# Optimization experiments

Measured on AMD Instinct MI355X. Metric: run time of the kernel, lower is better.

Reference implementation:

```python
import math
import jax, jax.numpy as jnp
import numpy as np

N, C_S, C_Z, C, H, PQK, PV = 768, 384, 128, 16, 12, 4, 8
INF, EPS = 100000.0, 1e-8


def _quat_to_rot(q):
    # q: [N,4] normalized quaternions -> [N,3,3] rotation matrices
    w, x, y, z = q[:, 0], q[:, 1], q[:, 2], q[:, 3]
    return jnp.stack([
        jnp.stack([1 - 2 * (y * y + z * z), 2 * (x * y - w * z), 2 * (x * z + w * y)], -1),
        jnp.stack([2 * (x * y + w * z), 1 - 2 * (x * x + z * z), 2 * (y * z - w * x)], -1),
        jnp.stack([2 * (x * z - w * y), 2 * (y * z + w * x), 1 - 2 * (x * x + y * y)], -1),
    ], -2)


def setup_inputs() -> dict:
    key = jax.random.key(0)
    ks = jax.random.split(key, 16)
    quat = jax.random.normal(ks[2], (N, 4))
    quat = quat / jnp.linalg.norm(quat, axis=-1, keepdims=True)
    sc = 0.02
    return {
        "s": jax.random.normal(ks[0], (N, C_S), jnp.float32),
        "z": jax.random.normal(ks[1], (N, N, C_Z), jnp.float32),
        "rot": _quat_to_rot(quat).astype(jnp.float32),
        "trans": jax.random.normal(ks[3], (N, 3), jnp.float32),
        "mask": jnp.ones((N,), jnp.float32),
        "Wq": sc * jax.random.normal(ks[4], (C_S, H * C), jnp.float32),
        "bq": jnp.zeros((H * C,), jnp.float32),
        "Wqp": sc * jax.random.normal(ks[5], (C_S, H * 3 * PQK), jnp.float32),
        "bqp": jnp.zeros((H * 3 * PQK,), jnp.float32),
        "Wkv": sc * jax.random.normal(ks[6], (C_S, 2 * H * C), jnp.float32),
        "bkv": jnp.zeros((2 * H * C,), jnp.float32),
        "Wkvp": sc * jax.random.normal(ks[7], (C_S, H * 3 * (PQK + PV)), jnp.float32),
        "bkvp": jnp.zeros((H * 3 * (PQK + PV),), jnp.float32),
        "Wb": sc * jax.random.normal(ks[8], (C_Z, H), jnp.float32),
        "bb": jnp.zeros((H,), jnp.float32),
        "head_weights": 0.5413 * jnp.ones((H,), jnp.float32),  # softplus^{-1}(1)
        "Wout": sc * jax.random.normal(ks[9], (H * (C_Z + C + PV * 4), C_S), jnp.float32),
        "bout": jnp.zeros((C_S,), jnp.float32),
    }


def _proj_points(x, W, b, rot, trans, P):
    # PointProjection: split last dim into 3 coord chunks, stack as last axis
    pl = x @ W + b                                   # [N, H*3*P]
    pl = pl.reshape(-1, 3, H * P).transpose(0, 2, 1).reshape(-1, H, P, 3)
    return jnp.einsum('nij,nhpj->nhpi', rot, pl) + trans[:, None, None, :]


def reference(s, z, rot, trans, mask, Wq, bq, Wqp, bqp, Wkv, bkv, Wkvp, bkvp,
              Wb, bb, head_weights, Wout, bout):
    q = (s @ Wq + bq).reshape(N, H, C)
    kv = (s @ Wkv + bkv).reshape(N, H, 2 * C)
    k, v = kv[..., :C], kv[..., C:]
    q_pts = _proj_points(s, Wqp, bqp, rot, trans, PQK)          # [N,H,PQK,3]
    kv_pts = _proj_points(s, Wkvp, bkvp, rot, trans, PQK + PV)  # [N,H,PQK+PV,3]
    k_pts, v_pts = kv_pts[..., :PQK, :], kv_pts[..., PQK:, :]

    b_bias = z @ Wb + bb                                        # [N,N,H]
    a = jnp.einsum('qhc,khc->hqk', q, k) * math.sqrt(1.0 / (3 * C))
    a = a + math.sqrt(1.0 / 3) * jnp.transpose(b_bias, (2, 0, 1))

    # point-distance attention: [q,k,H,PQK]
    d2 = jnp.sum((q_pts[:, None] - k_pts[None]) ** 2, axis=-1)
    hw = jax.nn.softplus(head_weights) * math.sqrt(1.0 / (3 * (PQK * 9.0 / 2)))
    pt_att = -0.5 * jnp.sum(d2 * hw[:, None], axis=-1)          # [q,k,H]
    a = a + jnp.transpose(pt_att, (2, 0, 1))

    sq_mask = INF * (mask[:, None] * mask[None, :] - 1.0)       # [q,k]
    a = jax.nn.softmax(a + sq_mask[None], axis=-1)              # [H,q,k]

    o = jnp.einsum('hqk,khc->qhc', a, v).reshape(N, H * C)
    o_pt = jnp.einsum('hqk,khpd->qhpd', a, v_pts)               # [q,H,PV,3]
    o_pt = jnp.einsum('nji,nhpj->nhpi', rot, o_pt - trans[:, None, None, :])  # invert_apply
    o_pt_norm = jnp.sqrt(jnp.sum(o_pt ** 2, -1) + EPS).reshape(N, H * PV)
    o_pt_flat = o_pt.reshape(N, H * PV, 3)
    o_pair = jnp.einsum('hqk,qkc->qhc', a, z).reshape(N, H * C_Z)

    cat = jnp.concatenate(
        [o, o_pt_flat[..., 0], o_pt_flat[..., 1], o_pt_flat[..., 2], o_pt_norm, o_pair], -1)
    return cat @ Wout + bout
```

## Files before the change

kernel.cpp:

```cpp
#include <hip/hip_runtime.h>
#include <math.h>

#define NN    768
#define CS    384
#define INF_  100000.0f

typedef __attribute__((ext_vector_type(8))) short s16x8;
typedef __attribute__((ext_vector_type(4))) float f32x4;

#define OFF_Q       0
#define OFF_K       147456
#define OFF_V       294912
#define OFF_QPRAW   442368
#define OFF_KVPRAW  552960
#define OFF_QPTS    884736
#define OFF_KPTS    995328
#define OFF_VPTS    1105920
#define OFF_KT      1327104
#define OFF_KPT     1474560
#define OFF_S       1585152
#define OFF_CAT     8414208

__device__ __forceinline__ unsigned short f2bf(float x) {
  unsigned u = __float_as_uint(x) + 0x8000u;
  return (unsigned short)(u >> 16);
}
__device__ __forceinline__ unsigned pk2(float a, float b) {
  return (unsigned)f2bf(a) | ((unsigned)f2bf(b) << 16);
}
__device__ __forceinline__ float bf2f(unsigned short u) {
  return __uint_as_float(((unsigned)u) << 16);
}

__global__ void __launch_bounds__(256)
k1_proj(const float* __restrict__ s,
        const float* __restrict__ Wq,  const float* __restrict__ bq,
        const float* __restrict__ Wqp, const float* __restrict__ bqp,
        const float* __restrict__ Wkv, const float* __restrict__ bkv,
        const float* __restrict__ Wkvp,const float* __restrict__ bkvp,
        float* __restrict__ ws) {
  const int n0 = blockIdx.x * 16;
  const int m0 = blockIdx.y * 128;
  const int t  = threadIdx.x;

  const float* W; const float* bv; int base, ncols;
  if (n0 < 192)      { W = Wq;   bv = bq;   base = 0;   ncols = 192; }
  else if (n0 < 576) { W = Wkv;  bv = bkv;  base = 192; ncols = 384; }
  else if (n0 < 720) { W = Wqp;  bv = bqp;  base = 576; ncols = 144; }
  else               { W = Wkvp; bv = bkvp; base = 720; ncols = 432; }
  const int jj0 = n0 - base;

  __shared__ float As[32 * 130];
  __shared__ float Bs[32 * 20];
  const int tx = t & 3, ty = t >> 2;
  float acc[2][4] = {{0.f}};

  for (int kc = 0; kc < CS; kc += 32) {
    __syncthreads();
    #pragma unroll
    for (int jj = 0; jj < 4; ++jj) {
      const int idx = t + 256 * jj;
      const int row = idx >> 3, c4 = idx & 7;
      const float4 v = *(const float4*)&s[(size_t)(m0 + row) * CS + kc + c4 * 4];
      As[(c4 * 4 + 0) * 130 + row] = v.x;
      As[(c4 * 4 + 1) * 130 + row] = v.y;
      As[(c4 * 4 + 2) * 130 + row] = v.z;
      As[(c4 * 4 + 3) * 130 + row] = v.w;
    }
    if (t < 128) {
      const int row = t >> 2, c4 = t & 3;
      const float4 v = *(const float4*)&W[(size_t)(kc + row) * ncols + jj0 + c4 * 4];
      *(float4*)&Bs[row * 20 + c4 * 4] = v;
    }
    __syncthreads();
    #pragma unroll 8
    for (int k = 0; k < 32; ++k) {
      const float2 a2 = *(const float2*)&As[k * 130 + ty * 2];
      const float4 b4 = *(const float4*)&Bs[k * 20 + tx * 4];
      acc[0][0] += a2.x * b4.x; acc[0][1] += a2.x * b4.y;
      acc[0][2] += a2.x * b4.z; acc[0][3] += a2.x * b4.w;
      acc[1][0] += a2.y * b4.x; acc[1][1] += a2.y * b4.y;
      acc[1][2] += a2.y * b4.z; acc[1][3] += a2.y * b4.w;
    }
  }

  #pragma unroll
  for (int r = 0; r < 2; ++r) {
    const int n = m0 + ty * 2 + r;
    #pragma unroll
    for (int e = 0; e < 4; ++e) {
      const int j = n0 + tx * 4 + e;
      const float val = acc[r][e] + bv[j - base];
      if (j < 192) {
        (ws + OFF_Q)[n * 192 + j] = val;
      } else if (j < 576) {
        const int jj = j - 192, h = jj >> 5, c = jj & 31;
        if (c < 16) (ws + OFF_K)[n * 192 + h * 16 + c] = val;
        else        (ws + OFF_V)[n * 192 + h * 16 + (c - 16)] = val;
      } else if (j < 720) {
        (ws + OFF_QPRAW)[n * 144 + (j - 576)] = val;
      } else {
        (ws + OFF_KVPRAW)[n * 432 + (j - 720)] = val;
      }
    }
  }
}

__global__ void __launch_bounds__(256)
k2_rot(const float* __restrict__ rot, const float* __restrict__ trans,
       float* __restrict__ ws) {
  const int idx = blockIdx.x * 256 + threadIdx.x;
  const int n = idx / 192;
  const int r = idx % 192;
  const float* R = rot + n * 9;
  const float* T = trans + n * 3;
  if (r < 48) {
    const float* raw = ws + OFF_QPRAW + n * 144;
    float p0 = raw[r], p1 = raw[48 + r], p2 = raw[96 + r];
    float g0 = R[0]*p0 + R[1]*p1 + R[2]*p2 + T[0];
    float g1 = R[3]*p0 + R[4]*p1 + R[5]*p2 + T[1];
    float g2 = R[6]*p0 + R[7]*p1 + R[8]*p2 + T[2];
    float* qp = ws + OFF_QPTS + n * 144 + r * 3;
    qp[0] = g0; qp[1] = g1; qp[2] = g2;
  } else {
    const int r2 = r - 48;
    const float* raw = ws + OFF_KVPRAW + n * 432;
    float p0 = raw[r2], p1 = raw[144 + r2], p2 = raw[288 + r2];
    float g0 = R[0]*p0 + R[1]*p1 + R[2]*p2 + T[0];
    float g1 = R[3]*p0 + R[4]*p1 + R[5]*p2 + T[1];
    float g2 = R[6]*p0 + R[7]*p1 + R[8]*p2 + T[2];
    const int h = r2 / 12, p = r2 % 12;
    if (p < 4) {
      float* kp = ws + OFF_KPTS + n * 144 + (h * 4 + p) * 3;
      kp[0] = g0; kp[1] = g1; kp[2] = g2;
    } else {
      float* vp = ws + OFF_VPTS + n * 288 + (h * 8 + (p - 4)) * 3;
      vp[0] = g0; vp[1] = g1; vp[2] = g2;
    }
  }
}

__global__ void __launch_bounds__(256)
k2b_tr(float* __restrict__ ws) {
  const int i = blockIdx.x * 256 + threadIdx.x;
  if (i < 147456) {
    const int n = i / 192, cc = i % 192;
    (ws + OFF_KT)[cc * 768 + n] = (ws + OFF_K)[i];
  } else {
    const int i2 = i - 147456;
    const int n = i2 / 144, r = i2 % 144;
    (ws + OFF_KPT)[r * 768 + n] = (ws + OFF_KPTS)[i2];
  }
}

__global__ void __launch_bounds__(256)
ks_scores(const float* __restrict__ mask, const float* __restrict__ bb,
          const float* __restrict__ hwin, float* __restrict__ ws) {
  const int k0 = blockIdx.x * 64;
  const int q0 = blockIdx.y * 16;
  const int t = threadIdx.x;
  const int g = t >> 6, kl = t & 63;
  const int kg = k0 + kl;

  const float* ktr  = ws + OFF_KT;
  const float* kptr = ws + OFF_KPT;
  float F[3][28];
  #pragma unroll
  for (int j = 0; j < 3; ++j) {
    const int h = g + 4 * j;
    #pragma unroll
    for (int c = 0; c < 16; ++c) F[j][c] = ktr[(h * 16 + c) * 768 + kg];
    #pragma unroll
    for (int r = 0; r < 12; ++r) F[j][16 + r] = kptr[(h * 12 + r) * 768 + kg];
  }
  float hw3[3], bb3[3];
  #pragma unroll
  for (int j = 0; j < 3; ++j) {
    const int h = g + 4 * j;
    hw3[j] = logf(1.0f + expf(hwin[h])) * 0.13608276348795434f;
    bb3[j] = 0.57735026918962576f * bb[h];
  }
  const float maskk = mask[kg];
  unsigned short* Sg = (unsigned short*)(ws + OFF_S);

  for (int qi = 0; qi < 16; ++qi) {
    const int q = q0 + qi;
    const float mterm = INF_ * (mask[q] * maskk - 1.0f);
    const float* qrow  = ws + OFF_Q    + q * 192;
    const float* qprow = ws + OFF_QPTS + q * 144;
    #pragma unroll
    for (int j = 0; j < 3; ++j) {
      const int h = g + 4 * j;
      float qk = 0.f;
      #pragma unroll
      for (int c = 0; c < 16; ++c) qk += qrow[h * 16 + c] * F[j][c];
      float pt = 0.f;
      #pragma unroll
      for (int r = 0; r < 12; ++r) {
        const float d = qprow[h * 12 + r] - F[j][16 + r];
        pt += d * d;
      }
      const float S = 0.14433756729740643f * qk - 0.5f * hw3[j] * pt
                    + bb3[j] + mterm;
      Sg[(size_t)(q * 12 + h) * 768 + kg] = f2bf(S);
    }
  }
}

#define ZT_S 72
#define ZR_S 136
#define WT_S 72
#define WH_S 68
__global__ void __launch_bounds__(256, 3)
k3_fused(const float* __restrict__ z, const float* __restrict__ rot,
         const float* __restrict__ trans, const float* __restrict__ Wb,
         float* __restrict__ ws) {
  const int q = blockIdx.x, t = threadIdx.x;
  const int g = t >> 6, kl = t & 63;
  const int l15 = kl & 15, lq = kl >> 4;

  __shared__ unsigned short zT[128 * ZT_S];
  __shared__ unsigned short zR[64 * ZR_S];
  __shared__ unsigned short wT[16 * WT_S];
  __shared__ float wH[12 * WH_S];
  __shared__ float bias_s[64 * 13];
  __shared__ float lsum[12], linv[12];
  __shared__ float opt_raw[288];

  s16x8 wbA[4];
  #pragma unroll
  for (int kk = 0; kk < 4; ++kk) {
    #pragma unroll
    for (int j = 0; j < 8; ++j) {
      float v = (l15 < 12) ? Wb[(kk * 32 + lq * 8 + j) * 12 + l15] : 0.0f;
      wbA[kk][j] = (short)f2bf(v);
    }
  }

  const float* vbase = ws + OFF_V;
  const float* vpbase= ws + OFF_VPTS;
  const unsigned short* Sg = (const unsigned short*)(ws + OFF_S);
  const float4* zg4  = (const float4*)z + (size_t)q * 24576;

  float l3[3] = {0.f, 0.f, 0.f};
  f32x4 opA = {0.f,0.f,0.f,0.f}, opB = {0.f,0.f,0.f,0.f};
  float o_acc = 0.f, pt0 = 0.f, pt1 = 0.f;
  const int oh = t >> 4;
  const int ph = t / 24;
  const int p2s = 256 + t, p2h = p2s / 24;

  for (int k0 = 0; k0 < NN; k0 += 64) {
    __syncthreads();

    const int kb = t >> 5, c4 = t & 31;
    #pragma unroll
    for (int half = 0; half < 2; ++half) {
      float4 zv[4];
      #pragma unroll
      for (int j = 0; j < 4; ++j)
        zv[j] = zg4[(size_t)(k0 + kb + 8 * (half * 4 + j)) * 32 + c4];
      #pragma unroll
      for (int j = 0; j < 4; ++j) {
        uint2 d;
        d.x = pk2(zv[j].x, zv[j].y);
        d.y = pk2(zv[j].z, zv[j].w);
        *(uint2*)&zR[(kb + 8 * (half * 4 + j)) * ZR_S + c4 * 4] = d;
      }
      #pragma unroll
      for (int w = 0; w < 4; ++w) {
        const int e = ((c4 >> 1) + w) & 3;
        uint2 d;
        d.x = pk2(((const float*)&zv[0])[e], ((const float*)&zv[1])[e]);
        d.y = pk2(((const float*)&zv[2])[e], ((const float*)&zv[3])[e]);
        *(uint2*)&zT[(c4 * 4 + e) * ZT_S + kb * 8 + half * 4] = d;
      }
    }
    __syncthreads();

    {
      f32x4 bd = {0.f,0.f,0.f,0.f};
      #pragma unroll
      for (int kk = 0; kk < 4; ++kk) {
        s16x8 bf = *(const s16x8*)&zR[(g * 16 + l15) * ZR_S + kk * 32 + lq * 8];
        bd = __builtin_amdgcn_mfma_f32_16x16x32_bf16(wbA[kk], bf, bd, 0, 0, 0);
      }
      #pragma unroll
      for (int r = 0; r < 4; ++r) {
        const int h = lq * 4 + r;
        if (h < 12) bias_s[(g * 16 + l15) * 13 + h] = bd[r];
      }
    }
    __syncthreads();

    {
      const int kg = k0 + kl;
      #pragma unroll
      for (int j = 0; j < 3; ++j) {
        const int h = g + 4 * j;
        const float Sv = bf2f(Sg[(size_t)(q * 12 + h) * 768 + kg]);
        const float wv = __expf(Sv + 0.57735026918962576f * bias_s[kl * 13 + h]);
        l3[j] += wv;
        wH[h * WH_S + kl] = wv;
        wT[h * WT_S + ((kl & 7) * 8 + (kl >> 3))] = f2bf(wv);
      }
    }
    __syncthreads();

    #pragma unroll
    for (int kk = 0; kk < 2; ++kk) {
      s16x8 af = *(const s16x8*)&wT[l15 * WT_S + kk * 32 + lq * 8];
      s16x8 b0 = *(const s16x8*)&zT[((2 * g)     * 16 + l15) * ZT_S + kk * 32 + lq * 8];
      opA = __builtin_amdgcn_mfma_f32_16x16x32_bf16(af, b0, opA, 0, 0, 0);
      s16x8 b1 = *(const s16x8*)&zT[((2 * g + 1) * 16 + l15) * ZT_S + kk * 32 + lq * 8];
      opB = __builtin_amdgcn_mfma_f32_16x16x32_bf16(af, b1, opB, 0, 0, 0);
    }
    {
      const float* vpr = vpbase + (size_t)k0 * 288;
      const float* vr  = vbase  + (size_t)k0 * 192;
      #pragma unroll 4
      for (int k4 = 0; k4 < 16; ++k4) {
        const int k = k4 * 4;
        {
          const float4 w4 = *(const float4*)&wH[ph * WH_S + k];
          pt0 += w4.x * vpr[(k    ) * 288 + t] + w4.y * vpr[(k + 1) * 288 + t]
               + w4.z * vpr[(k + 2) * 288 + t] + w4.w * vpr[(k + 3) * 288 + t];
        }
        if (t < 32) {
          const float4 w4 = *(const float4*)&wH[p2h * WH_S + k];
          pt1 += w4.x * vpr[(k    ) * 288 + p2s] + w4.y * vpr[(k + 1) * 288 + p2s]
               + w4.z * vpr[(k + 2) * 288 + p2s] + w4.w * vpr[(k + 3) * 288 + p2s];
        }
        if (t < 192) {
          const float4 w4 = *(const float4*)&wH[oh * WH_S + k];
          o_acc += w4.x * vr[(k    ) * 192 + t] + w4.y * vr[(k + 1) * 192 + t]
                 + w4.z * vr[(k + 2) * 192 + t] + w4.w * vr[(k + 3) * 192 + t];
        }
      }
    }
  }

  #pragma unroll
  for (int j = 0; j < 3; ++j) {
    float v = l3[j];
    for (int off = 1; off < 64; off <<= 1) v += __shfl_xor(v, off, 64);
    l3[j] = v;
  }
  if (kl == 0) { lsum[g] = l3[0]; lsum[g + 4] = l3[1]; lsum[g + 8] = l3[2]; }
  __syncthreads();
  if (t < 12) linv[t] = 1.0f / lsum[t];
  __syncthreads();

  float* cat = ws + OFF_CAT + (size_t)q * 2112;
  #pragma unroll
  for (int r = 0; r < 4; ++r) {
    const int h = lq * 4 + r;
    if (h < 12) {
      cat[576 + h * 128 + (2 * g)     * 16 + l15] = opA[r] * linv[h];
      cat[576 + h * 128 + (2 * g + 1) * 16 + l15] = opB[r] * linv[h];
    }
  }
  if (t < 192) cat[t] = o_acc * linv[oh];
  opt_raw[t] = pt0 * linv[ph];
  if (t < 32) opt_raw[p2s] = pt1 * linv[p2h];
  __syncthreads();

  if (t < 96) {
    const int h = t >> 3, p = t & 7;
    const float* R = rot + q * 9;
    const float* T = trans + q * 3;
    const float g0 = opt_raw[h * 24 + p * 3 + 0] - T[0];
    const float g1 = opt_raw[h * 24 + p * 3 + 1] - T[1];
    const float g2 = opt_raw[h * 24 + p * 3 + 2] - T[2];
    const float x  = R[0]*g0 + R[3]*g1 + R[6]*g2;
    const float y  = R[1]*g0 + R[4]*g1 + R[7]*g2;
    const float zc = R[2]*g0 + R[5]*g1 + R[8]*g2;
    const int hp = h * 8 + p;
    cat[192 + hp] = x;
    cat[288 + hp] = y;
    cat[384 + hp] = zc;
    cat[480 + hp] = sqrtf(x*x + y*y + zc*zc + 1e-8f);
  }
}

__global__ void __launch_bounds__(256)
k5_init(const float* __restrict__ bout, float* __restrict__ out) {
  const int i = blockIdx.x * 256 + threadIdx.x;
  out[i] = bout[i % 384];
}

__global__ void __launch_bounds__(256)
k5_out(const float* __restrict__ Wout, const float* __restrict__ ws,
       float* __restrict__ out) {
  const int n0  = blockIdx.x * 64;
  const int m0  = blockIdx.y * 64;
  const int ks0 = blockIdx.z * 352;
  const int t = threadIdx.x;

  __shared__ float As[32 * 68];
  __shared__ float Bs[32 * 68];
  const int tx = t & 15, ty = t >> 4;
  float acc[4][4] = {{0.f}};

  const float* catg = ws + OFF_CAT;
  for (int kc = 0; kc < 352; kc += 32) {
    __syncthreads();
    #pragma unroll
    for (int p = 0; p < 2; ++p) {
      const int idx = t + 256 * p;
      const int m = idx >> 3, c4 = idx & 7;
      const float4 v = *(const float4*)&catg[(size_t)(m0 + m) * 2112 + ks0 + kc + c4 * 4];
      As[(c4 * 4 + 0) * 68 + m] = v.x;
      As[(c4 * 4 + 1) * 68 + m] = v.y;
      As[(c4 * 4 + 2) * 68 + m] = v.z;
      As[(c4 * 4 + 3) * 68 + m] = v.w;
    }
    #pragma unroll
    for (int p = 0; p < 8; ++p) {
      const int idx = t + 256 * p;
      const int k = idx >> 6, n = idx & 63;
      Bs[k * 68 + n] = Wout[(size_t)(ks0 + kc + k) * 384 + n0 + n];
    }
    __syncthreads();
    #pragma unroll 8
    for (int k = 0; k < 32; ++k) {
      const float4 a4 = *(const float4*)&As[k * 68 + ty * 4];
      const float4 b4 = *(const float4*)&Bs[k * 68 + tx * 4];
      acc[0][0] += a4.x * b4.x; acc[0][1] += a4.x * b4.y; acc[0][2] += a4.x * b4.z; acc[0][3] += a4.x * b4.w;
      acc[1][0] += a4.y * b4.x; acc[1][1] += a4.y * b4.y; acc[1][2] += a4.y * b4.z; acc[1][3] += a4.y * b4.w;
      acc[2][0] += a4.z * b4.x; acc[2][1] += a4.z * b4.y; acc[2][2] += a4.z * b4.z; acc[2][3] += a4.z * b4.w;
      acc[3][0] += a4.w * b4.x; acc[3][1] += a4.w * b4.y; acc[3][2] += a4.w * b4.z; acc[3][3] += a4.w * b4.w;
    }
  }
  #pragma unroll
  for (int r = 0; r < 4; ++r)
    #pragma unroll
    for (int c = 0; c < 4; ++c)
      atomicAdd(&out[(size_t)(m0 + ty * 4 + r) * 384 + n0 + tx * 4 + c], acc[r][c]);
}

extern "C" void kernel_launch(void* const* d_in, const int* in_sizes, int n_in,
                              void* d_out, int out_size, void* d_ws, size_t ws_size,
                              hipStream_t stream) {
  const float* s     = (const float*)d_in[0];
  const float* z     = (const float*)d_in[1];
  const float* rot   = (const float*)d_in[2];
  const float* trans = (const float*)d_in[3];
  const float* mask  = (const float*)d_in[4];
  const float* Wq    = (const float*)d_in[5];
  const float* bq    = (const float*)d_in[6];
  const float* Wqp   = (const float*)d_in[7];
  const float* bqp   = (const float*)d_in[8];
  const float* Wkv   = (const float*)d_in[9];
  const float* bkv   = (const float*)d_in[10];
  const float* Wkvp  = (const float*)d_in[11];
  const float* bkvp  = (const float*)d_in[12];
  const float* Wb    = (const float*)d_in[13];
  const float* bb    = (const float*)d_in[14];
  const float* hw    = (const float*)d_in[15];
  const float* Wout  = (const float*)d_in[16];
  const float* bout  = (const float*)d_in[17];
  float* out = (float*)d_out;
  float* ws  = (float*)d_ws;

  k1_proj<<<dim3(72, 6), 256, 0, stream>>>(s, Wq, bq, Wqp, bqp, Wkv, bkv, Wkvp, bkvp, ws);
  k2_rot <<<576, 256, 0, stream>>>(rot, trans, ws);
  k2b_tr <<<1008, 256, 0, stream>>>(ws);
  ks_scores<<<dim3(12, 48), 256, 0, stream>>>(mask, bb, hw, ws);
  k3_fused<<<NN, 256, 0, stream>>>(z, rot, trans, Wb, ws);
  k5_init<<<1152, 256, 0, stream>>>(bout, out);
  k5_out<<<dim3(6, 12, 6), 256, 0, stream>>>(Wout, ws, out);
}
```

Measured before the change: 734.6 us.

## Prefetch next z tile and scores into registers; use LDS-only barriers

```diff
diff --git a/kernel.cpp b/kernel.cpp
--- a/kernel.cpp
+++ b/kernel.cpp
@@ -31,6 +31,11 @@
 __device__ __forceinline__ float bf2f(unsigned short u) {
   return __uint_as_float(((unsigned)u) << 16);
 }
+
+#define LDS_BARRIER() do { \
+  asm volatile("s_waitcnt lgkmcnt(0)" ::: "memory"); \
+  __builtin_amdgcn_s_barrier(); \
+} while (0)
 
 __global__ void __launch_bounds__(256)
 k1_proj(const float* __restrict__ s,
@@ -249,33 +254,52 @@
   const int ph = t / 24;
   const int p2s = 256 + t, p2h = p2s / 24;
 
+  const int kb = t >> 5, c4 = t & 31;
+
+  float4 zv[8];
+  #pragma unroll
+  for (int m = 0; m < 8; ++m)
+    zv[m] = zg4[(size_t)(kb + 8 * m) * 32 + c4];
+  unsigned short Sn[3];
+  #pragma unroll
+  for (int j = 0; j < 3; ++j)
+    Sn[j] = Sg[(size_t)(q * 12 + (g + 4 * j)) * 768 + kl];
+
   for (int k0 = 0; k0 < NN; k0 += 64) {
-    __syncthreads();
-
-    const int kb = t >> 5, c4 = t & 31;
+    LDS_BARRIER();
+
     #pragma unroll
     for (int half = 0; half < 2; ++half) {
-      float4 zv[4];
-      #pragma unroll
-      for (int j = 0; j < 4; ++j)
-        zv[j] = zg4[(size_t)(k0 + kb + 8 * (half * 4 + j)) * 32 + c4];
       #pragma unroll
       for (int j = 0; j < 4; ++j) {
+        const float4 v = zv[half * 4 + j];
         uint2 d;
-        d.x = pk2(zv[j].x, zv[j].y);
-        d.y = pk2(zv[j].z, zv[j].w);
+        d.x = pk2(v.x, v.y);
+        d.y = pk2(v.z, v.w);
         *(uint2*)&zR[(kb + 8 * (half * 4 + j)) * ZR_S + c4 * 4] = d;
       }
       #pragma unroll
       for (int w = 0; w < 4; ++w) {
         const int e = ((c4 >> 1) + w) & 3;
         uint2 d;
-        d.x = pk2(((const float*)&zv[0])[e], ((const float*)&zv[1])[e]);
-        d.y = pk2(((const float*)&zv[2])[e], ((const float*)&zv[3])[e]);
+        d.x = pk2(((const float*)&zv[half * 4 + 0])[e], ((const float*)&zv[half * 4 + 1])[e]);
+        d.y = pk2(((const float*)&zv[half * 4 + 2])[e], ((const float*)&zv[half * 4 + 3])[e]);
         *(uint2*)&zT[(c4 * 4 + e) * ZT_S + kb * 8 + half * 4] = d;
       }
     }
-    __syncthreads();
+    unsigned short Scur[3];
+    #pragma unroll
+    for (int j = 0; j < 3; ++j) Scur[j] = Sn[j];
+    LDS_BARRIER();
+
+    if (k0 + 64 < NN) {
+      #pragma unroll
+      for (int m = 0; m < 8; ++m)
+        zv[m] = zg4[(size_t)(k0 + 64 + kb + 8 * m) * 32 + c4];
+      #pragma unroll
+      for (int j = 0; j < 3; ++j)
+        Sn[j] = Sg[(size_t)(q * 12 + (g + 4 * j)) * 768 + k0 + 64 + kl];
+    }
 
     {
       f32x4 bd = {0.f,0.f,0.f,0.f};
@@ -290,21 +314,20 @@
         if (h < 12) bias_s[(g * 16 + l15) * 13 + h] = bd[r];
       }
     }
-    __syncthreads();
+    LDS_BARRIER();
 
     {
-      const int kg = k0 + kl;
       #pragma unroll
       for (int j = 0; j < 3; ++j) {
         const int h = g + 4 * j;
-        const float Sv = bf2f(Sg[(size_t)(q * 12 + h) * 768 + kg]);
+        const float Sv = bf2f(Scur[j]);
         const float wv = __expf(Sv + 0.57735026918962576f * bias_s[kl * 13 + h]);
         l3[j] += wv;
         wH[h * WH_S + kl] = wv;
         wT[h * WT_S + ((kl & 7) * 8 + (kl >> 3))] = f2bf(wv);
       }
     }
-    __syncthreads();
+    LDS_BARRIER();
 
     #pragma unroll
     for (int kk = 0; kk < 2; ++kk) {
```

New measurement: 764.9 us. +4.1%, slower.

## Compute attention-weighted V and V-point sums with bf16 MFMA from pre-packed matrix

Applied to the files above, without the earlier changes.

```diff
diff --git a/kernel.cpp b/kernel.cpp
--- a/kernel.cpp
+++ b/kernel.cpp
@@ -19,6 +19,7 @@
 #define OFF_KT      1327104
 #define OFF_KPT     1474560
 #define OFF_S       1585152
+#define OFF_MT      5124096
 #define OFF_CAT     8414208
 
 __device__ __forceinline__ unsigned short f2bf(float x) {
@@ -146,10 +147,23 @@
   if (i < 147456) {
     const int n = i / 192, cc = i % 192;
     (ws + OFF_KT)[cc * 768 + n] = (ws + OFF_K)[i];
-  } else {
+  } else if (i < 258048) {
     const int i2 = i - 147456;
     const int n = i2 / 144, r = i2 % 144;
     (ws + OFF_KPT)[r * 768 + n] = (ws + OFF_KPTS)[i2];
+  } else {
+    const int im = i - 258048;
+    const int row = im / 768, p = im - row * 768;
+    unsigned short* M = (unsigned short*)(ws + OFF_MT);
+    float val = 0.0f;
+    if (row < 480) {
+      const int hh = row / 40, c = row - hh * 40;
+      const int pl = p & 63;
+      const int k = (p & ~63) | (((pl & 7) << 3) | (pl >> 3));
+      val = (c < 16) ? (ws + OFF_V)[k * 192 + hh * 16 + c]
+                     : (ws + OFF_VPTS)[k * 288 + hh * 24 + (c - 16)];
+    }
+    M[row * 768 + p] = f2bf(val);
   }
 }
 
@@ -210,7 +224,6 @@
 #define ZT_S 72
 #define ZR_S 136
 #define WT_S 72
-#define WH_S 68
 __global__ void __launch_bounds__(256, 3)
 k3_fused(const float* __restrict__ z, const float* __restrict__ rot,
          const float* __restrict__ trans, const float* __restrict__ Wb,
@@ -222,7 +235,6 @@
   __shared__ unsigned short zT[128 * ZT_S];
   __shared__ unsigned short zR[64 * ZR_S];
   __shared__ unsigned short wT[16 * WT_S];
-  __shared__ float wH[12 * WH_S];
   __shared__ float bias_s[64 * 13];
   __shared__ float lsum[12], linv[12];
   __shared__ float opt_raw[288];
@@ -237,41 +249,47 @@
     }
   }
 
-  const float* vbase = ws + OFF_V;
-  const float* vpbase= ws + OFF_VPTS;
   const unsigned short* Sg = (const unsigned short*)(ws + OFF_S);
   const float4* zg4  = (const float4*)z + (size_t)q * 24576;
+  const unsigned short* mbase = (const unsigned short*)(ws + OFF_MT)
+                              + (size_t)(g * 128 + l15) * 768 + lq * 8;
 
   float l3[3] = {0.f, 0.f, 0.f};
   f32x4 opA = {0.f,0.f,0.f,0.f}, opB = {0.f,0.f,0.f,0.f};
-  float o_acc = 0.f, pt0 = 0.f, pt1 = 0.f;
-  const int oh = t >> 4;
-  const int ph = t / 24;
-  const int p2s = 256 + t, p2h = p2s / 24;
+  f32x4 acc[8];
+  #pragma unroll
+  for (int i = 0; i < 8; ++i) acc[i] = (f32x4){0.f,0.f,0.f,0.f};
+
+  const int kb = t >> 5, c4 = t & 31;
 
   for (int k0 = 0; k0 < NN; k0 += 64) {
     __syncthreads();
 
-    const int kb = t >> 5, c4 = t & 31;
+    float4 zv[8];
+    #pragma unroll
+    for (int m = 0; m < 8; ++m)
+      zv[m] = zg4[(size_t)(k0 + kb + 8 * m) * 32 + c4];
+    unsigned short Sc[3];
+    #pragma unroll
+    for (int j = 0; j < 3; ++j)
+      Sc[j] = Sg[(size_t)(q * 12 + (g + 4 * j)) * 768 + k0 + kl];
+
     #pragma unroll
     for (int half = 0; half < 2; ++half) {
-      float4 zv[4];
-      #pragma unroll
-      for (int j = 0; j < 4; ++j)
-        zv[j] = zg4[(size_t)(k0 + kb + 8 * (half * 4 + j)) * 32 + c4];
       #pragma unroll
       for (int j = 0; j < 4; ++j) {
+        const float4 v = zv[half * 4 + j];
         uint2 d;
-        d.x = pk2(zv[j].x, zv[j].y);
-        d.y = pk2(zv[j].z, zv[j].w);
+        d.x = pk2(v.x, v.y);
+        d.y = pk2(v.z, v.w);
         *(uint2*)&zR[(kb + 8 * (half * 4 + j)) * ZR_S + c4 * 4] = d;
       }
       #pragma unroll
       for (int w = 0; w < 4; ++w) {
         const int e = ((c4 >> 1) + w) & 3;
         uint2 d;
-        d.x = pk2(((const float*)&zv[0])[e], ((const float*)&zv[1])[e]);
-        d.y = pk2(((const float*)&zv[2])[e], ((const float*)&zv[3])[e]);
+        d.x = pk2(((const float*)&zv[half * 4 + 0])[e], ((const float*)&zv[half * 4 + 1])[e]);
+        d.y = pk2(((const float*)&zv[half * 4 + 2])[e], ((const float*)&zv[half * 4 + 3])[e]);
         *(uint2*)&zT[(c4 * 4 + e) * ZT_S + kb * 8 + half * 4] = d;
       }
     }
@@ -293,48 +311,38 @@
     __syncthreads();
 
     {
-      const int kg = k0 + kl;
       #pragma unroll
       for (int j = 0; j < 3; ++j) {
         const int h = g + 4 * j;
-        const float Sv = bf2f(Sg[(size_t)(q * 12 + h) * 768 + kg]);
+        const float Sv = bf2f(Sc[j]);
         const float wv = __expf(Sv + 0.57735026918962576f * bias_s[kl * 13 + h]);
         l3[j] += wv;
-        wH[h * WH_S + kl] = wv;
         wT[h * WT_S + ((kl & 7) * 8 + (kl >> 3))] = f2bf(wv);
       }
     }
     __syncthreads();
 
-    #pragma unroll
-    for (int kk = 0; kk < 2; ++kk) {
-      s16x8 af = *(const s16x8*)&wT[l15 * WT_S + kk * 32 + lq * 8];
-      s16x8 b0 = *(const s16x8*)&zT[((2 * g)     * 16 + l15) * ZT_S + kk * 32 + lq * 8];
-      opA = __builtin_amdgcn_mfma_f32_16x16x32_bf16(af, b0, opA, 0, 0, 0);
-      s16x8 b1 = *(const s16x8*)&zT[((2 * g + 1) * 16 + l15) * ZT_S + kk * 32 + lq * 8];
-      opB = __builtin_amdgcn_mfma_f32_16x16x32_bf16(af, b1, opB, 0, 0, 0);
-    }
+    const s16x8 af0 = *(const s16x8*)&wT[l15 * WT_S + lq * 8];
+    const s16x8 af1 = *(const s16x8*)&wT[l15 * WT_S + 32 + lq * 8];
     {
-      const float* vpr = vpbase + (size_t)k0 * 288;
-      const float* vr  = vbase  + (size_t)k0 * 192;
-      #pragma unroll 4
-      for (int k4 = 0; k4 < 16; ++k4) {
-        const int k = k4 * 4;
-        {
-          const float4 w4 = *(const float4*)&wH[ph * WH_S + k];
-          pt0 += w4.x * vpr[(k    ) * 288 + t] + w4.y * vpr[(k + 1) * 288 + t]
-               + w4.z * vpr[(k + 2) * 288 + t] + w4.w * vpr[(k + 3) * 288 + t];
-        }
-        if (t < 32) {
-          const float4 w4 = *(const float4*)&wH[p2h * WH_S + k];
-          pt1 += w4.x * vpr[(k    ) * 288 + p2s] + w4.y * vpr[(k + 1) * 288 + p2s]
-               + w4.z * vpr[(k + 2) * 288 + p2s] + w4.w * vpr[(k + 3) * 288 + p2s];
-        }
-        if (t < 192) {
-          const float4 w4 = *(const float4*)&wH[oh * WH_S + k];
-          o_acc += w4.x * vr[(k    ) * 192 + t] + w4.y * vr[(k + 1) * 192 + t]
-                 + w4.z * vr[(k + 2) * 192 + t] + w4.w * vr[(k + 3) * 192 + t];
-        }
+      s16x8 b0 = *(const s16x8*)&zT[((2 * g)     * 16 + l15) * ZT_S + lq * 8];
+      s16x8 b1 = *(const s16x8*)&zT[((2 * g)     * 16 + l15) * ZT_S + 32 + lq * 8];
+      s16x8 b2 = *(const s16x8*)&zT[((2 * g + 1) * 16 + l15) * ZT_S + lq * 8];
+      s16x8 b3 = *(const s16x8*)&zT[((2 * g + 1) * 16 + l15) * ZT_S + 32 + lq * 8];
+      opA = __builtin_amdgcn_mfma_f32_16x16x32_bf16(af0, b0, opA, 0, 0, 0);
+      opA = __builtin_amdgcn_mfma_f32_16x16x32_bf16(af1, b1, opA, 0, 0, 0);
+      opB = __builtin_amdgcn_mfma_f32_16x16x32_bf16(af0, b2, opB, 0, 0, 0);
+      opB = __builtin_amdgcn_mfma_f32_16x16x32_bf16(af1, b3, opB, 0, 0, 0);
+    }
+    {
+      const unsigned short* mp = mbase + k0;
+      #pragma unroll
+      for (int ti = 0; ti < 8; ++ti) {
+        const s16x8 m0 = *(const s16x8*)(mp);
+        const s16x8 m1 = *(const s16x8*)(mp + 32);
+        acc[ti] = __builtin_amdgcn_mfma_f32_16x16x32_bf16(af0, m0, acc[ti], 0, 0, 0);
+        acc[ti] = __builtin_amdgcn_mfma_f32_16x16x32_bf16(af1, m1, acc[ti], 0, 0, 0);
+        mp += 16 * 768;
       }
     }
   }
@@ -351,6 +359,7 @@
   __syncthreads();
 
   float* cat = ws + OFF_CAT + (size_t)q * 2112;
+
   #pragma unroll
   for (int r = 0; r < 4; ++r) {
     const int h = lq * 4 + r;
@@ -359,9 +368,21 @@
       cat[576 + h * 128 + (2 * g + 1) * 16 + l15] = opB[r] * linv[h];
     }
   }
-  if (t < 192) cat[t] = o_acc * linv[oh];
-  opt_raw[t] = pt0 * linv[ph];
-  if (t < 32) opt_raw[p2s] = pt1 * linv[p2h];
+
+  #pragma unroll
+  for (int ti = 0; ti < 8; ++ti) {
+    const int cg = (g * 8 + ti) * 16 + l15;
+    const int hh = cg / 40;
+    const int c  = cg - hh * 40;
+    #pragma unroll
+    for (int r = 0; r < 4; ++r) {
+      if (hh < 12 && (lq * 4 + r) == hh) {
+        const float val = acc[ti][r] * linv[hh];
+        if (c < 16) cat[hh * 16 + c] = val;
+        else        opt_raw[hh * 24 + (c - 16)] = val;
+      }
+    }
+  }
   __syncthreads();
 
   if (t < 96) {
@@ -464,7 +485,7 @@
 
   k1_proj<<<dim3(72, 6), 256, 0, stream>>>(s, Wq, bq, Wqp, bqp, Wkv, bkv, Wkvp, bkvp, ws);
   k2_rot <<<576, 256, 0, stream>>>(rot, trans, ws);
-  k2b_tr <<<1008, 256, 0, stream>>>(ws);
+  k2b_tr <<<2544, 256, 0, stream>>>(ws);
   ks_scores<<<dim3(12, 48), 256, 0, stream>>>(mask, bb, hw, ws);
   k3_fused<<<NN, 256, 0, stream>>>(z, rot, trans, Wb, ws);
   k5_init<<<1152, 256, 0, stream>>>(bout, out);
```

Result: faster. 713.9 us (-2.8%).
